# Optimization experiments

Measured on AMD Instinct MI355X. Metric: run time of the kernel, lower is better.

## Reference

```python
import jax, jax.numpy as jnp
import numpy as np

E, D, H, O, K = 12, 1024, 2048, 1024, 4
HH, G1, G2 = H // 2, 256, 128
B = 4096


def _ln(x, g, b):
    # torch LayerNorm over last dim, eps=1e-5
    m = x.mean(-1, keepdims=True)
    v = ((x - m) ** 2).mean(-1, keepdims=True)
    return (x - m) * jax.lax.rsqrt(v + 1e-5) * g + b


def setup_inputs() -> dict:
    key = jax.random.key(0)
    ks = jax.random.split(key, 12)
    s = 0.02
    f32 = jnp.float32
    return {
        "x": jax.random.normal(ks[0], (B, D), f32),
        # stacked expert params (E experts)
        "ew_in": jax.random.normal(ks[1], (E, D, H), f32) * s,
        "eb_in": jnp.full((E, H), 0.1, f32),
        "ln1_g": jnp.ones((E, H), f32),
        "ln1_b": jnp.zeros((E, H), f32),
        "ew_h1": jax.random.normal(ks[2], (E, H, H), f32) * s,
        "eb_h1": jnp.full((E, H), 0.1, f32),
        "ln2_g": jnp.ones((E, H), f32),
        "ln2_b": jnp.zeros((E, H), f32),
        "ew_h2": jax.random.normal(ks[3], (E, H, HH), f32) * s,
        "eb_h2": jnp.full((E, HH), 0.1, f32),
        "ew_out": jax.random.normal(ks[4], (E, HH, O), f32) * s,
        "eb_out": jnp.zeros((E, O), f32),
        # gating network params
        "gw_in": jax.random.normal(ks[5], (D, G1), f32) * s,
        "gb_in": jnp.zeros((G1,), f32),
        "gln1_g": jnp.ones((G1,), f32),
        "gln1_b": jnp.zeros((G1,), f32),
        "gw_1": jax.random.normal(ks[6], (G1, G1), f32) * s,
        "gb_1": jnp.full((G1,), 0.1, f32),
        "gln2_g": jnp.ones((G1,), f32),
        "gln2_b": jnp.zeros((G1,), f32),
        "gw_2": jax.random.normal(ks[7], (G1, G2), f32) * s,
        "gb_2": jnp.full((G2,), 0.1, f32),
        "gw_out": jax.random.normal(ks[8], (G2, E), f32) * s,
        "gb_out": jnp.zeros((E,), f32),
        "temperature": jnp.ones((1,), f32),
    }


def _moe(x, ew_in, eb_in, ln1_g, ln1_b, ew_h1, eb_h1, ln2_g, ln2_b, ew_h2,
         eb_h2, ew_out, eb_out, gw_in, gb_in, gln1_g, gln1_b, gw_1, gb_1,
         gln2_g, gln2_b, gw_2, gb_2, gw_out, gb_out, temperature):
    # ---- gating network (eval mode: no dropout / noise) ----
    g0 = jax.nn.relu(x @ gw_in + gb_in)                                # [B,256]
    g1 = jax.nn.relu(_ln(g0, gln1_g, gln1_b)) @ gw_1 + gb_1 + g0       # residual
    g2 = jax.nn.relu(_ln(g1, gln2_g, gln2_b)) @ gw_2 + gb_2            # [B,128]
    logits = (g2 @ gw_out + gb_out) / temperature                      # [B,E]
    probs = jax.nn.softmax(logits, axis=1)
    topp, topi = jax.lax.top_k(probs, K)                               # [B,K]
    topp = topp / topp.sum(axis=1, keepdims=True)
    # ---- experts: batched over E, combined with top-k one-hot weights ----
    h0 = jax.nn.relu(jnp.einsum('bd,edh->ebh', x, ew_in) + eb_in[:, None, :])
    a1 = jax.nn.relu(_ln(h0, ln1_g[:, None, :], ln1_b[:, None, :]))
    h1 = jnp.einsum('ebh,ehg->ebg', a1, ew_h1) + eb_h1[:, None, :] + h0
    a2 = jax.nn.silu(_ln(h1, ln2_g[:, None, :], ln2_b[:, None, :]))
    h2 = jnp.einsum('ebh,ehm->ebm', a2, ew_h2) + eb_h2[:, None, :]     # [E,B,H/2]
    y = jnp.einsum('ebm,emo->ebo', h2, ew_out) + eb_out[:, None, :]    # [E,B,O]
    oh = jax.nn.one_hot(topi, E, dtype=probs.dtype)                    # [B,K,E]
    w = jnp.einsum('bk,bke->be', topp, oh)                             # combine weights
    final = jnp.einsum('be,ebo->bo', w, y)                             # [B,O]
    # ---- load-balancing loss (eval-mode path) ----
    usage = probs.mean(axis=0)                                         # [E]
    ideal = 1.0 / E
    kl = jnp.sum(ideal * (jnp.log(ideal) - jnp.log(usage + 1e-8)))
    var = jnp.sum((usage - ideal) ** 2)
    ent = -jnp.sum(usage * jnp.log(usage + 1e-8))
    ent_loss = 1.0 - ent / np.log(E).astype(np.float32)
    loss = (0.5 * kl + 0.3 * var + 0.2 * ent_loss) * 0.05
    return final, loss, probs


def reference(x, ew_in, eb_in, ln1_g, ln1_b, ew_h1, eb_h1, ln2_g, ln2_b,
              ew_h2, eb_h2, ew_out, eb_out, gw_in, gb_in, gln1_g, gln1_b,
              gw_1, gb_1, gln2_g, gln2_b, gw_2, gb_2, gw_out, gb_out,
              temperature):
    return _moe(x, ew_in, eb_in, ln1_g, ln1_b, ew_h1, eb_h1, ln2_g, ln2_b,
                ew_h2, eb_h2, ew_out, eb_out, gw_in, gb_in, gln1_g, gln1_b,
                gw_1, gb_1, gln2_g, gln2_b, gw_2, gb_2, gw_out, gb_out,
                temperature)
```

## Files before the change

### kernel.cpp

```cpp
#include <hip/hip_runtime.h>
#include <cstdint>
#include <cstddef>

typedef __bf16 bf16;
typedef __bf16 bf16x4 __attribute__((ext_vector_type(4)));
typedef __bf16 bf16x8 __attribute__((ext_vector_type(8)));
typedef float  f32x4  __attribute__((ext_vector_type(4)));

#define NE   12
#define DDIM 1024
#define HDIM 2048
#define MDIM 1024
#define ODIM 1024
#define GG1  256
#define GG2  128
#define BB   4096
#define ROWS_MAX 18432

#define GPTR(p) ((const __attribute__((address_space(1))) void*)(p))
#define LPTR(p) ((__attribute__((address_space(3))) void*)(p))

__global__ void cvt_f32_bf16(const float* __restrict__ in, bf16* __restrict__ out) {
    size_t i = ((size_t)blockIdx.x * 256 + threadIdx.x) * 4;
    float4 v = *(const float4*)(in + i);
    bf16x4 o = { (bf16)v.x, (bf16)v.y, (bf16)v.z, (bf16)v.w };
    *(bf16x4*)(out + i) = o;
}

__global__ void transpose_cvt(const float* __restrict__ in, bf16* __restrict__ out,
                              int K, int N) {
    __shared__ float tile[32][33];
    const size_t eo = (size_t)blockIdx.z * K * N;
    in  += eo;
    out += eo;
    const int n0 = blockIdx.x * 32, k0 = blockIdx.y * 32;
    const int tx = threadIdx.x, ty = threadIdx.y;
    #pragma unroll
    for (int i = 0; i < 4; ++i)
        tile[ty + i * 8][tx] = in[(size_t)(k0 + ty + i * 8) * N + n0 + tx];
    __syncthreads();
    #pragma unroll
    for (int i = 0; i < 4; ++i)
        out[(size_t)(n0 + ty + i * 8) * K + k0 + tx] = (bf16)tile[tx][ty + i * 8];
}

__global__ void route_init(int* __restrict__ tok2slot, int* __restrict__ lists,
                           int* __restrict__ counts, int* __restrict__ cursors) {
    const int i = blockIdx.x * 256 + threadIdx.x;
    if (i < BB * NE)   tok2slot[i] = -1;
    if (i < ROWS_MAX)  lists[i] = 0;
    if (i < NE)        { counts[i] = 0; cursors[i] = 0; }
}

__global__ void route_count(const float* __restrict__ wcomb, int* __restrict__ counts) {
    const int t = blockIdx.x * 256 + threadIdx.x;
    const int e = blockIdx.y;
    if (wcomb[(size_t)t * NE + e] > 0.f) atomicAdd(&counts[e], 1);
}

__global__ void route_offsets(const int* __restrict__ counts, int* __restrict__ offs) {
    if (threadIdx.x == 0) {
        int o = 0;
        for (int e = 0; e < NE; ++e) { offs[e] = o; o += (counts[e] + 127) & ~127; }
        offs[NE] = o;
    }
}

__global__ void route_assign(const float* __restrict__ wcomb, const int* __restrict__ offs,
                             int* __restrict__ cursors, int* __restrict__ lists,
                             int* __restrict__ tok2slot) {
    const int t = blockIdx.x * 256 + threadIdx.x;
    const int e = blockIdx.y;
    if (wcomb[(size_t)t * NE + e] > 0.f) {
        const int pos  = atomicAdd(&cursors[e], 1);
        const int slot = offs[e] + pos;
        lists[slot] = t;
        tok2slot[(size_t)t * NE + e] = slot;
    }
}

__global__ void gather_rows(const bf16* __restrict__ xb, const int* __restrict__ lists,
                            const int* __restrict__ offs, bf16* __restrict__ xg) {
    const int e = blockIdx.y, p = blockIdx.x;
    const int off = offs[e];
    if (p >= offs[e + 1] - off) return;
    const int slot = off + p;
    const int t = lists[slot];
    const int tid = threadIdx.x;
    *(bf16x8*)&xg[(size_t)slot * DDIM + tid * 8] =
        *(const bf16x8*)&xb[(size_t)t * DDIM + tid * 8];
}

__global__ void combine_out(const int* __restrict__ tok2slot, const float* __restrict__ wcomb,
                            const float* __restrict__ yc, float* __restrict__ out) {
    const int t = blockIdx.x, tid = threadIdx.x;
    float4 acc = { 0.f, 0.f, 0.f, 0.f };
    #pragma unroll
    for (int e = 0; e < NE; ++e) {
        const int s = tok2slot[(size_t)t * NE + e];
        if (s >= 0) {
            const float w = wcomb[(size_t)t * NE + e];
            const float4 y = *(const float4*)&yc[(size_t)s * ODIM + tid * 4];
            acc.x += w * y.x; acc.y += w * y.y; acc.z += w * y.z; acc.w += w * y.w;
        }
    }
    *(float4*)&out[(size_t)t * ODIM + tid * 4] = acc;
}

template<int EPI>
__global__ __launch_bounds__(256, 2)
void egemm(const bf16* __restrict__ A, const bf16* __restrict__ Wt,
           const float* __restrict__ bias, const bf16* __restrict__ res,
           bf16* __restrict__ Cb, float* __restrict__ Cf,
           const int* __restrict__ offs, int N, int K)
{
    const int e = blockIdx.z;
    const int off  = offs[e];
    const int cntp = offs[e + 1] - off;
    const int m0 = blockIdx.y * 128;
    if (m0 >= cntp) return;
    const int n0 = blockIdx.x * 128;

    __shared__ bf16 sA[2][128 * 32];
    __shared__ bf16 sB[2][128 * 32];
    const int tid  = threadIdx.x;
    const int lane = tid & 63;
    const int wave = tid >> 6;
    const int wr = wave >> 1, wc = wave & 1;
    const int q  = lane >> 4;
    const int lr = lane & 15;

    const bf16*  Ae  = A + (size_t)off * K;
    const bf16*  Wte = Wt + (size_t)e * N * K;
    const float* be  = bias + (size_t)e * N;

    const bf16* srcA[2];
    const bf16* srcB[2];
    int dsto[2];
    #pragma unroll
    for (int i = 0; i < 2; ++i) {
        const int ch  = i * 256 + tid;
        const int row = ch >> 2, c = ch & 3;
        const int qg  = c ^ ((row >> 1) & 3);
        srcA[i] = Ae  + (size_t)(m0 + row) * K + qg * 8;
        srcB[i] = Wte + (size_t)(n0 + row) * K + qg * 8;
        dsto[i] = (i * 256 + (tid & 192)) * 8;
    }

    f32x4 acc[4][4] = {};

    auto stage = [&](int buf, int k0) {
        #pragma unroll
        for (int i = 0; i < 2; ++i) {
            __builtin_amdgcn_global_load_lds(GPTR(srcA[i] + k0), LPTR(&sA[buf][dsto[i]]), 16, 0, 0);
            __builtin_amdgcn_global_load_lds(GPTR(srcB[i] + k0), LPTR(&sB[buf][dsto[i]]), 16, 0, 0);
        }
    };

    stage(0, 0);
    __syncthreads();

    const int NT = K >> 5;
    int cur = 0;
    for (int kt = 0; kt < NT; ++kt) {
        if (kt + 1 < NT) stage(cur ^ 1, (kt + 1) << 5);
        bf16x8 fa[4], fb[4];
        #pragma unroll
        for (int mi = 0; mi < 4; ++mi) {
            const int r = wr * 64 + mi * 16 + lr;
            const int c = q ^ ((r >> 1) & 3);
            fa[mi] = *(const bf16x8*)&sA[cur][(size_t)(r * 4 + c) * 8];
        }
        #pragma unroll
        for (int ni = 0; ni < 4; ++ni) {
            const int r = wc * 64 + ni * 16 + lr;
            const int c = q ^ ((r >> 1) & 3);
            fb[ni] = *(const bf16x8*)&sB[cur][(size_t)(r * 4 + c) * 8];
        }
        #pragma unroll
        for (int mi = 0; mi < 4; ++mi)
            #pragma unroll
            for (int ni = 0; ni < 4; ++ni)
                acc[mi][ni] = __builtin_amdgcn_mfma_f32_16x16x32_bf16(fa[mi], fb[ni], acc[mi][ni], 0, 0, 0);
        __syncthreads();
        cur ^= 1;
    }

    #pragma unroll
    for (int ni = 0; ni < 4; ++ni) {
        const int c  = n0 + wc * 64 + ni * 16 + lr;
        const float bv = be[c];
        #pragma unroll
        for (int mi = 0; mi < 4; ++mi) {
            const int rloc = wr * 64 + mi * 16 + q * 4;
            #pragma unroll
            for (int j = 0; j < 4; ++j) {
                const size_t idx = (size_t)(off + m0 + rloc + j) * N + c;
                float v = acc[mi][ni][j] + bv;
                if constexpr (EPI == 0)      { Cb[idx] = (bf16)fmaxf(v, 0.f); }
                else if constexpr (EPI == 1) { Cb[idx] = (bf16)(v + (float)res[idx]); }
                else if constexpr (EPI == 2) { Cb[idx] = (bf16)v; }
                else                         { Cf[idx] = v; }
            }
        }
    }
}

template<int ACT>
__global__ __launch_bounds__(256)
void ln_act_bf16(const bf16* __restrict__ in, const float* __restrict__ gam,
                 const float* __restrict__ bet, bf16* __restrict__ out,
                 const int* __restrict__ offs)
{
    const int e = blockIdx.y;
    const int row = blockIdx.x;
    const int off = offs[e];
    if (row >= offs[e + 1] - off) return;
    const int tid = threadIdx.x;
    const size_t base = (size_t)(off + row) * HDIM;
    const float* g = gam + (size_t)e * HDIM;
    const float* b = bet + (size_t)e * HDIM;
    bf16x8 v = *(const bf16x8*)(in + base + tid * 8);
    float x[8], s = 0.f, ss = 0.f;
    #pragma unroll
    for (int j = 0; j < 8; ++j) { x[j] = (float)v[j]; s += x[j]; ss += x[j] * x[j]; }
    #pragma unroll
    for (int o = 1; o < 64; o <<= 1) { s += __shfl_xor(s, o); ss += __shfl_xor(ss, o); }
    __shared__ float rs[4], rss[4];
    if ((tid & 63) == 0) { rs[tid >> 6] = s; rss[tid >> 6] = ss; }
    __syncthreads();
    s  = rs[0] + rs[1] + rs[2] + rs[3];
    ss = rss[0] + rss[1] + rss[2] + rss[3];
    const float mean = s * (1.f / HDIM);
    const float var  = ss * (1.f / HDIM) - mean * mean;
    const float rstd = rsqrtf(var + 1e-5f);
    bf16x8 ov;
    #pragma unroll
    for (int j = 0; j < 8; ++j) {
        const int col = tid * 8 + j;
        float y = (x[j] - mean) * rstd * g[col] + b[col];
        if constexpr (ACT == 0) y = fmaxf(y, 0.f);
        else                    y = y / (1.f + expf(-y));
        ov[j] = (bf16)y;
    }
    *(bf16x8*)(out + base + tid * 8) = ov;
}

template<int EPI>
__global__ __launch_bounds__(256)
void gemm_f32(const float* __restrict__ A, const float* __restrict__ Bm,
              const float* __restrict__ bias, const float* __restrict__ res,
              float* __restrict__ C, int M, int N, int K)
{
    __shared__ float As[64][17];
    __shared__ float Bs[16][64];
    const int tid = threadIdx.x;
    const int tx = tid & 15, ty = tid >> 4;
    const int n0 = blockIdx.x * 64, m0 = blockIdx.y * 64;
    float acc[4][4] = {};

    for (int k0 = 0; k0 < K; k0 += 16) {
        {
            const int r = tid >> 2, c = (tid & 3) * 4;
            const float4 va = *(const float4*)(A + (size_t)(m0 + r) * K + k0 + c);
            As[r][c] = va.x; As[r][c + 1] = va.y; As[r][c + 2] = va.z; As[r][c + 3] = va.w;
            const int rb = tid >> 4, cb = (tid & 15) * 4;
            *(float4*)&Bs[rb][cb] = *(const float4*)(Bm + (size_t)(k0 + rb) * N + n0 + cb);
        }
        __syncthreads();
        #pragma unroll
        for (int k = 0; k < 16; ++k) {
            const float4 b4 = *(const float4*)&Bs[k][tx * 4];
            float av[4];
            #pragma unroll
            for (int i = 0; i < 4; ++i) av[i] = As[ty * 4 + i][k];
            #pragma unroll
            for (int i = 0; i < 4; ++i) {
                acc[i][0] += av[i] * b4.x; acc[i][1] += av[i] * b4.y;
                acc[i][2] += av[i] * b4.z; acc[i][3] += av[i] * b4.w;
            }
        }
        __syncthreads();
    }

    const float4 b4 = *(const float4*)(bias + n0 + tx * 4);
    #pragma unroll
    for (int i = 0; i < 4; ++i) {
        const int r = m0 + ty * 4 + i;
        float o[4] = { acc[i][0] + b4.x, acc[i][1] + b4.y, acc[i][2] + b4.z, acc[i][3] + b4.w };
        if constexpr (EPI == 0) {
            #pragma unroll
            for (int j = 0; j < 4; ++j) o[j] = fmaxf(o[j], 0.f);
        } else if constexpr (EPI == 1) {
            const float4 r4 = *(const float4*)(res + (size_t)r * N + n0 + tx * 4);
            o[0] += r4.x; o[1] += r4.y; o[2] += r4.z; o[3] += r4.w;
        }
        float4 o4 = { o[0], o[1], o[2], o[3] };
        *(float4*)(C + (size_t)r * N + n0 + tx * 4) = o4;
    }
}

__global__ void ln_relu_f32_256(const float* __restrict__ in, const float* __restrict__ g,
                                const float* __restrict__ b, float* __restrict__ out)
{
    const int row = blockIdx.x, lane = threadIdx.x;
    const size_t base = (size_t)row * GG1;
    const float4 v = *(const float4*)(in + base + lane * 4);
    float s  = v.x + v.y + v.z + v.w;
    float ss = v.x * v.x + v.y * v.y + v.z * v.z + v.w * v.w;
    #pragma unroll
    for (int o = 1; o < 64; o <<= 1) { s += __shfl_xor(s, o); ss += __shfl_xor(ss, o); }
    const float mean = s * (1.f / GG1);
    const float var  = ss * (1.f / GG1) - mean * mean;
    const float rstd = rsqrtf(var + 1e-5f);
    const float4 g4 = *(const float4*)(g + lane * 4);
    const float4 b4 = *(const float4*)(b + lane * 4);
    float4 o4;
    o4.x = fmaxf((v.x - mean) * rstd * g4.x + b4.x, 0.f);
    o4.y = fmaxf((v.y - mean) * rstd * g4.y + b4.y, 0.f);
    o4.z = fmaxf((v.z - mean) * rstd * g4.z + b4.z, 0.f);
    o4.w = fmaxf((v.w - mean) * rstd * g4.w + b4.w, 0.f);
    *(float4*)(out + base + lane * 4) = o4;
}

__global__ void gate_head(const float* __restrict__ g2, const float* __restrict__ gwout,
                          const float* __restrict__ gbout, const float* __restrict__ temp,
                          float* __restrict__ probs_out, float* __restrict__ wout)
{
    const int row = blockIdx.x, lane = threadIdx.x;
    __shared__ float lg[NE];
    const int e = lane >> 2, part = lane & 3;
    float acc = 0.f;
    if (e < NE) {
        const float* gr = g2 + (size_t)row * GG2;
        #pragma unroll
        for (int i = 0; i < 32; ++i) {
            const int k = part * 32 + i;
            acc += gr[k] * gwout[(size_t)k * NE + e];
        }
    }
    acc += __shfl_xor(acc, 1);
    acc += __shfl_xor(acc, 2);
    if (e < NE && part == 0) lg[e] = acc + gbout[e];
    __syncthreads();
    if (lane == 0) {
        const float t = temp[0];
        float p[NE];
        float mx = -1e30f;
        #pragma unroll
        for (int i = 0; i < NE; ++i) { p[i] = lg[i] / t; mx = fmaxf(mx, p[i]); }
        float se = 0.f;
        #pragma unroll
        for (int i = 0; i < NE; ++i) { p[i] = expf(p[i] - mx); se += p[i]; }
        const float inv = 1.f / se;
        #pragma unroll
        for (int i = 0; i < NE; ++i) { p[i] *= inv; probs_out[(size_t)row * NE + i] = p[i]; }
        float qq[NE], w[NE];
        #pragma unroll
        for (int i = 0; i < NE; ++i) { qq[i] = p[i]; w[i] = 0.f; }
        float tv[4]; int ti[4]; float tsum = 0.f;
        for (int k = 0; k < 4; ++k) {
            int best = 0; float bv = qq[0];
            for (int i = 1; i < NE; ++i) if (qq[i] > bv) { bv = qq[i]; best = i; }
            tv[k] = bv; ti[k] = best; qq[best] = -1e30f; tsum += bv;
        }
        const float it = 1.f / tsum;
        for (int k = 0; k < 4; ++k) w[ti[k]] = tv[k] * it;
        #pragma unroll
        for (int i = 0; i < NE; ++i) wout[(size_t)row * NE + i] = w[i];
    }
}

__global__ void usage_mean(const float* __restrict__ probs, float* __restrict__ usage) {
    const int e = blockIdx.x, tid = threadIdx.x;
    float s = 0.f;
    for (int r = tid; r < BB; r += 256) s += probs[(size_t)r * NE + e];
    #pragma unroll
    for (int o = 1; o < 64; o <<= 1) s += __shfl_xor(s, o);
    __shared__ float ps[4];
    if ((tid & 63) == 0) ps[tid >> 6] = s;
    __syncthreads();
    if (tid == 0) usage[e] = (ps[0] + ps[1] + ps[2] + ps[3]) / (float)BB;
}

__global__ void loss_kernel(const float* __restrict__ usage, float* __restrict__ out_loss) {
    if (threadIdx.x == 0) {
        const float ideal = 1.f / 12.f;
        float kl = 0.f, var = 0.f, ent = 0.f;
        for (int e = 0; e < NE; ++e) {
            const float u = usage[e];
            kl  += ideal * (logf(ideal) - logf(u + 1e-8f));
            var += (u - ideal) * (u - ideal);
            ent -= u * logf(u + 1e-8f);
        }
        const float entl = 1.f - ent / logf(12.f);
        out_loss[0] = (0.5f * kl + 0.3f * var + 0.2f * entl) * 0.05f;
    }
}

extern "C" void kernel_launch(void* const* d_in, const int* in_sizes, int n_in,
                              void* d_out, int out_size, void* d_ws, size_t ws_size,
                              hipStream_t stream)
{
    const float* x      = (const float*)d_in[0];
    const float* ew_in  = (const float*)d_in[1];
    const float* eb_in  = (const float*)d_in[2];
    const float* ln1_g  = (const float*)d_in[3];
    const float* ln1_b  = (const float*)d_in[4];
    const float* ew_h1  = (const float*)d_in[5];
    const float* eb_h1  = (const float*)d_in[6];
    const float* ln2_g  = (const float*)d_in[7];
    const float* ln2_b  = (const float*)d_in[8];
    const float* ew_h2  = (const float*)d_in[9];
    const float* eb_h2  = (const float*)d_in[10];
    const float* ew_out = (const float*)d_in[11];
    const float* eb_out = (const float*)d_in[12];
    const float* gw_in  = (const float*)d_in[13];
    const float* gb_in  = (const float*)d_in[14];
    const float* gln1_g = (const float*)d_in[15];
    const float* gln1_b = (const float*)d_in[16];
    const float* gw_1   = (const float*)d_in[17];
    const float* gb_1   = (const float*)d_in[18];
    const float* gln2_g = (const float*)d_in[19];
    const float* gln2_b = (const float*)d_in[20];
    const float* gw_2   = (const float*)d_in[21];
    const float* gb_2   = (const float*)d_in[22];
    const float* gw_out = (const float*)d_in[23];
    const float* gb_out = (const float*)d_in[24];
    const float* temp   = (const float*)d_in[25];

    float* out_final = (float*)d_out;
    float* out_loss  = out_final + (size_t)BB * ODIM;
    float* out_probs = out_loss + 1;

    char* ws = (char*)d_ws;
    size_t off = 0;
    auto alloc = [&](size_t bytes) -> void* {
        void* p = ws + off;
        off += (bytes + 255) & ~(size_t)255;
        return p;
    };

    bf16* xb     = (bf16*)alloc((size_t)BB * DDIM * 2);
    bf16* wt_in  = (bf16*)alloc((size_t)NE * HDIM * DDIM * 2);
    bf16* wt_h1  = (bf16*)alloc((size_t)NE * HDIM * HDIM * 2);
    bf16* wt_h2  = (bf16*)alloc((size_t)NE * MDIM * HDIM * 2);
    bf16* wt_out = (bf16*)alloc((size_t)NE * ODIM * MDIM * 2);
    bf16* xg     = (bf16*)alloc((size_t)ROWS_MAX * DDIM * 2);
    bf16* regA   = (bf16*)alloc((size_t)ROWS_MAX * HDIM * 2);
    bf16* regB   = (bf16*)alloc((size_t)ROWS_MAX * HDIM * 2);
    bf16* h1     = (bf16*)alloc((size_t)ROWS_MAX * HDIM * 2);
    float* yc    = (float*)alloc((size_t)ROWS_MAX * ODIM * 4);
    bf16* h0 = regA; bf16* a2 = regA;
    bf16* a1 = regB; bf16* h2 = regB;
    float* g0    = (float*)alloc((size_t)BB * GG1 * 4);
    float* t1    = (float*)alloc((size_t)BB * GG1 * 4);
    float* g1    = (float*)alloc((size_t)BB * GG1 * 4);
    float* t2    = (float*)alloc((size_t)BB * GG1 * 4);
    float* g2b   = (float*)alloc((size_t)BB * GG2 * 4);
    float* wcomb = (float*)alloc((size_t)BB * NE * 4);
    int*   lists = (int*)alloc((size_t)ROWS_MAX * 4);
    int*   t2s   = (int*)alloc((size_t)BB * NE * 4);
    int*   counts= (int*)alloc(256);
    int*   curs  = (int*)alloc(256);
    int*   offs  = (int*)alloc(256);
    float* usage = (float*)alloc(256);

    cvt_f32_bf16<<<dim3(BB * DDIM / 1024), dim3(256), 0, stream>>>(x, xb);
    transpose_cvt<<<dim3(HDIM / 32, DDIM / 32, NE), dim3(32, 8), 0, stream>>>(ew_in,  wt_in,  DDIM, HDIM);
    transpose_cvt<<<dim3(HDIM / 32, HDIM / 32, NE), dim3(32, 8), 0, stream>>>(ew_h1,  wt_h1,  HDIM, HDIM);
    transpose_cvt<<<dim3(MDIM / 32, HDIM / 32, NE), dim3(32, 8), 0, stream>>>(ew_h2,  wt_h2,  HDIM, MDIM);
    transpose_cvt<<<dim3(ODIM / 32, MDIM / 32, NE), dim3(32, 8), 0, stream>>>(ew_out, wt_out, MDIM, ODIM);

    gemm_f32<0><<<dim3(GG1 / 64, BB / 64), dim3(256), 0, stream>>>(x,  gw_in, gb_in, nullptr, g0,  BB, GG1, DDIM);
    ln_relu_f32_256<<<dim3(BB), dim3(64), 0, stream>>>(g0, gln1_g, gln1_b, t1);
    gemm_f32<1><<<dim3(GG1 / 64, BB / 64), dim3(256), 0, stream>>>(t1, gw_1,  gb_1,  g0,      g1,  BB, GG1, GG1);
    ln_relu_f32_256<<<dim3(BB), dim3(64), 0, stream>>>(g1, gln2_g, gln2_b, t2);
    gemm_f32<2><<<dim3(GG2 / 64, BB / 64), dim3(256), 0, stream>>>(t2, gw_2,  gb_2,  nullptr, g2b, BB, GG2, GG1);
    gate_head<<<dim3(BB), dim3(64), 0, stream>>>(g2b, gw_out, gb_out, temp, out_probs, wcomb);
    usage_mean<<<dim3(NE), dim3(256), 0, stream>>>(out_probs, usage);
    loss_kernel<<<dim3(1), dim3(64), 0, stream>>>(usage, out_loss);

    route_init<<<dim3((BB * NE + 255) / 256), dim3(256), 0, stream>>>(t2s, lists, counts, curs);
    route_count<<<dim3(BB / 256, NE), dim3(256), 0, stream>>>(wcomb, counts);
    route_offsets<<<dim3(1), dim3(64), 0, stream>>>(counts, offs);
    route_assign<<<dim3(BB / 256, NE), dim3(256), 0, stream>>>(wcomb, offs, curs, lists, t2s);
    gather_rows<<<dim3(BB, NE), dim3(128), 0, stream>>>(xb, lists, offs, xg);

    egemm<0><<<dim3(HDIM / 128, BB / 128, NE), dim3(256), 0, stream>>>(
        xg, wt_in, eb_in, nullptr, h0, nullptr, offs, HDIM, DDIM);
    ln_act_bf16<0><<<dim3(BB, NE), dim3(256), 0, stream>>>(h0, ln1_g, ln1_b, a1, offs);
    egemm<1><<<dim3(HDIM / 128, BB / 128, NE), dim3(256), 0, stream>>>(
        a1, wt_h1, eb_h1, h0, h1, nullptr, offs, HDIM, HDIM);
    ln_act_bf16<1><<<dim3(BB, NE), dim3(256), 0, stream>>>(h1, ln2_g, ln2_b, a2, offs);
    egemm<2><<<dim3(MDIM / 128, BB / 128, NE), dim3(256), 0, stream>>>(
        a2, wt_h2, eb_h2, nullptr, h2, nullptr, offs, MDIM, HDIM);
    egemm<3><<<dim3(ODIM / 128, BB / 128, NE), dim3(256), 0, stream>>>(
        h2, wt_out, eb_out, nullptr, nullptr, yc, offs, ODIM, MDIM);

    combine_out<<<dim3(BB), dim3(256), 0, stream>>>(t2s, wcomb, yc, out_final);
}
```

Measured before the change: 981.1 us.

## Triple-buffer expert GEMM loads and widen weight transpose tiles

The expert GEMM now uses three LDS buffers, keeping two k-tiles in flight. Each iteration waits with an explicit vmcnt and one barrier, replacing the double-buffer scheme that had a full __syncthreads per iteration. This aims to hide global-to-LDS latency better, at the cost of more shared memory per block, which may reduce occupancy. Separately, the weight transpose-convert kernel moves to 64x64 tiles with float4 reads and 8-wide bf16 writes to cut memory transactions.

```diff
diff --git a/kernel.cpp b/kernel.cpp
--- a/kernel.cpp
+++ b/kernel.cpp
@@ -27,21 +27,35 @@
     *(bf16x4*)(out + i) = o;
 }
 
-__global__ void transpose_cvt(const float* __restrict__ in, bf16* __restrict__ out,
-                              int K, int N) {
-    __shared__ float tile[32][33];
+__global__ __launch_bounds__(256)
+void transpose_cvt(const float* __restrict__ in, bf16* __restrict__ out,
+                   int K, int N) {
+    __shared__ float tile[64][65];
     const size_t eo = (size_t)blockIdx.z * K * N;
     in  += eo;
     out += eo;
-    const int n0 = blockIdx.x * 32, k0 = blockIdx.y * 32;
-    const int tx = threadIdx.x, ty = threadIdx.y;
-    #pragma unroll
-    for (int i = 0; i < 4; ++i)
-        tile[ty + i * 8][tx] = in[(size_t)(k0 + ty + i * 8) * N + n0 + tx];
+    const int n0 = blockIdx.x * 64, k0 = blockIdx.y * 64;
+    const int tid = threadIdx.x;
+
+    const int rkk = tid >> 4, rnc = (tid & 15) * 4;
+    #pragma unroll
+    for (int p = 0; p < 4; ++p) {
+        const int kk = p * 16 + rkk;
+        const float4 v = *(const float4*)(in + (size_t)(k0 + kk) * N + n0 + rnc);
+        tile[kk][rnc] = v.x; tile[kk][rnc + 1] = v.y;
+        tile[kk][rnc + 2] = v.z; tile[kk][rnc + 3] = v.w;
+    }
     __syncthreads();
-    #pragma unroll
-    for (int i = 0; i < 4; ++i)
-        out[(size_t)(n0 + ty + i * 8) * K + k0 + tx] = (bf16)tile[tx][ty + i * 8];
+
+    const int wnn = tid >> 3, wkc = (tid & 7) * 8;
+    #pragma unroll
+    for (int p = 0; p < 2; ++p) {
+        const int nn = p * 32 + wnn;
+        bf16x8 o;
+        #pragma unroll
+        for (int j = 0; j < 8; ++j) o[j] = (bf16)tile[wkc + j][nn];
+        *(bf16x8*)(out + (size_t)(n0 + nn) * K + k0 + wkc) = o;
+    }
 }
 
 __global__ void route_init(int* __restrict__ tok2slot, int* __restrict__ lists,
@@ -121,8 +135,8 @@
     if (m0 >= cntp) return;
     const int n0 = blockIdx.x * 128;
 
-    __shared__ bf16 sA[2][128 * 32];
-    __shared__ bf16 sB[2][128 * 32];
+    __shared__ bf16 sA[3][128 * 32];
+    __shared__ bf16 sB[3][128 * 32];
     const int tid  = threadIdx.x;
     const int lane = tid & 63;
     const int wave = tid >> 6;
@@ -149,7 +163,8 @@
 
     f32x4 acc[4][4] = {};
 
-    auto stage = [&](int buf, int k0) {
+    auto stage = [&](int buf, int kt) {
+        const int k0 = kt << 5;
         #pragma unroll
         for (int i = 0; i < 2; ++i) {
             __builtin_amdgcn_global_load_lds(GPTR(srcA[i] + k0), LPTR(&sA[buf][dsto[i]]), 16, 0, 0);
@@ -157,13 +172,18 @@
         }
     };
 
+    const int NT = K >> 5;
     stage(0, 0);
-    __syncthreads();
-
-    const int NT = K >> 5;
-    int cur = 0;
+    stage(1, 1);
+
     for (int kt = 0; kt < NT; ++kt) {
-        if (kt + 1 < NT) stage(cur ^ 1, (kt + 1) << 5);
+        const int cur = kt % 3;
+        if (kt + 1 < NT) { asm volatile("s_waitcnt vmcnt(4)" ::: "memory"); }
+        else             { asm volatile("s_waitcnt vmcnt(0)" ::: "memory"); }
+        __builtin_amdgcn_sched_barrier(0);
+        __builtin_amdgcn_s_barrier();
+        __builtin_amdgcn_sched_barrier(0);
+
         bf16x8 fa[4], fb[4];
         #pragma unroll
         for (int mi = 0; mi < 4; ++mi) {
@@ -182,8 +202,8 @@
             #pragma unroll
             for (int ni = 0; ni < 4; ++ni)
                 acc[mi][ni] = __builtin_amdgcn_mfma_f32_16x16x32_bf16(fa[mi], fb[ni], acc[mi][ni], 0, 0, 0);
-        __syncthreads();
-        cur ^= 1;
+
+        if (kt + 2 < NT) stage((kt + 2) % 3, kt + 2);
     }
 
     #pragma unroll
@@ -467,10 +487,10 @@
     float* usage = (float*)alloc(256);
 
     cvt_f32_bf16<<<dim3(BB * DDIM / 1024), dim3(256), 0, stream>>>(x, xb);
-    transpose_cvt<<<dim3(HDIM / 32, DDIM / 32, NE), dim3(32, 8), 0, stream>>>(ew_in,  wt_in,  DDIM, HDIM);
-    transpose_cvt<<<dim3(HDIM / 32, HDIM / 32, NE), dim3(32, 8), 0, stream>>>(ew_h1,  wt_h1,  HDIM, HDIM);
-    transpose_cvt<<<dim3(MDIM / 32, HDIM / 32, NE), dim3(32, 8), 0, stream>>>(ew_h2,  wt_h2,  HDIM, MDIM);
-    transpose_cvt<<<dim3(ODIM / 32, MDIM / 32, NE), dim3(32, 8), 0, stream>>>(ew_out, wt_out, MDIM, ODIM);
+    transpose_cvt<<<dim3(HDIM / 64, DDIM / 64, NE), dim3(256), 0, stream>>>(ew_in,  wt_in,  DDIM, HDIM);
+    transpose_cvt<<<dim3(HDIM / 64, HDIM / 64, NE), dim3(256), 0, stream>>>(ew_h1,  wt_h1,  HDIM, HDIM);
+    transpose_cvt<<<dim3(MDIM / 64, HDIM / 64, NE), dim3(256), 0, stream>>>(ew_h2,  wt_h2,  HDIM, MDIM);
+    transpose_cvt<<<dim3(ODIM / 64, MDIM / 64, NE), dim3(256), 0, stream>>>(ew_out, wt_out, MDIM, ODIM);
 
     gemm_f32<0><<<dim3(GG1 / 64, BB / 64), dim3(256), 0, stream>>>(x,  gw_in, gb_in, nullptr, g0,  BB, GG1, DDIM);
     ln_relu_f32_256<<<dim3(BB), dim3(64), 0, stream>>>(g0, gln1_g, gln1_b, t1);
```

Measured after the change: 896.6 us. 1.09x faster.
